# Performance work log

Hardware: AMD Instinct MI355X
Metric: run time of the kernel (lower is better)

The kernel has to match this reference:

```python
import jax, jax.numpy as jnp
import numpy as np

HEADS = 4


def _forward(x_atoms, pos, edge_attr, molecular_features, emb_W, emb_b, mp_W1, mp_b1, mp_W2, mp_b2, ln_g, ln_b, attn_in_w, attn_in_b, attn_out_w, attn_out_b, pool_W, pool_b, mol_gate, lrn_gate, molemb_W1, molemb_b1, molemb_W2, molemb_b2, lrnemb_W1, lrnemb_b1, lrnemb_W2, lrnemb_b2, fus_W1, fus_b1, fus_W2, fus_b2, head_W1, head_b1, head_W2, head_b2, edge_index, batch_idx):
    N = x_atoms.shape[0]
    B = molecular_features.shape[0]
    A = N // B  # equal-size molecules; batch_idx = repeat(arange(B), A)
    H = emb_W.shape[1]
    L = mp_W1.shape[0]
    src, dst = edge_index[0], edge_index[1]  # PyG: x_j = x[src], x_i = x[dst]
    x = x_atoms @ emb_W + emb_b
    # distance features (constant across layers)
    diff = pos[dst] - pos[src]
    d = jnp.sqrt(jnp.sum(diff * diff, axis=1, keepdims=True) + 1e-12)
    dist_feat = jnp.concatenate([d, 1.0 / (1.0 + d), jnp.exp(-d)], axis=1)  # [E,3]
    ones_e = jnp.ones((src.shape[0], 1), x.dtype)
    cnt = jnp.maximum(jax.ops.segment_sum(ones_e, dst, num_segments=N), 1.0)
    for l in range(L):
        res = x
        msg = jnp.concatenate([x[dst], x[src], dist_feat], axis=1)  # [E, 2H+3]
        msg = jax.nn.relu(msg @ mp_W1[l] + mp_b1[l]) @ mp_W2[l] + mp_b2[l]
        x = jax.ops.segment_sum(msg, dst, num_segments=N) / cnt  # mean aggregation
        y = x + res
        mu = y.mean(-1, keepdims=True)
        var = jnp.var(y, axis=-1, keepdims=True)
        x = (y - mu) * jax.lax.rsqrt(var + 1e-5) * ln_g[l] + ln_b[l]
    xm = x.reshape(B, A, H)
    explicit = xm.mean(axis=1)  # scatter_mean over equal-size graphs
    # per-molecule multi-head self-attention (torch MHA, eval mode)
    hd = H // HEADS
    qkv = xm @ attn_in_w.T + attn_in_b
    q, k, v = jnp.split(qkv, 3, axis=-1)
    q = q.reshape(B, A, HEADS, hd)
    k = k.reshape(B, A, HEADS, hd)
    v = v.reshape(B, A, HEADS, hd)
    scores = jnp.einsum('bqhd,bkhd->bhqk', q, k) / jnp.sqrt(jnp.asarray(hd, x.dtype))
    att = jax.nn.softmax(scores, axis=-1)
    o = jnp.einsum('bhqk,bkhd->bqhd', att, v).reshape(B, A, H)
    attended = o @ attn_out_w.T + attn_out_b
    aw = jax.nn.softmax(jnp.sum(attended * xm, axis=-1), axis=1)  # [B,A]
    wmean = jnp.sum(attended * aw[..., None], axis=1)
    maxp = attended.max(axis=1)
    meanp = attended.mean(axis=1)
    stdp = jnp.std(attended, axis=1, ddof=1)  # torch.std unbiased
    pooled = jnp.stack([wmean, maxp, meanp, stdp], axis=0)  # [4,B,H]
    proj = jnp.einsum('kbh,khf->kbf', pooled, pool_W) + pool_b[:, None, :]
    learned = jnp.moveaxis(proj, 0, 1).reshape(B, -1)  # [B,LF]
    # per-property gated MLPs, vectorized over P (atom gates are computed but unused in the source)
    gm = molecular_features[None] * jax.nn.sigmoid(mol_gate)[:, None, :]
    gl = learned[None] * jax.nn.sigmoid(lrn_gate)[:, None, :]
    molrep = jax.nn.relu(jnp.einsum('pbm,pmh->pbh', gm, molemb_W1) + molemb_b1[:, None, :])
    molrep = jnp.einsum('pbh,phk->pbk', molrep, molemb_W2) + molemb_b2[:, None, :]
    lrnrep = jax.nn.relu(jnp.einsum('pbm,pmh->pbh', gl, lrnemb_W1) + lrnemb_b1[:, None, :])
    lrnrep = jnp.einsum('pbh,phk->pbk', lrnrep, lrnemb_W2) + lrnemb_b2[:, None, :]
    P = mol_gate.shape[0]
    comb = jnp.concatenate([jnp.broadcast_to(explicit[None], (P, B, H)), molrep, lrnrep], axis=-1)
    fused = jax.nn.relu(jnp.einsum('pbc,pch->pbh', comb, fus_W1) + fus_b1[:, None, :])
    fused = jnp.einsum('pbh,phk->pbk', fused, fus_W2) + fus_b2[:, None, :]
    h = jax.nn.relu(jnp.einsum('pbh,phk->pbk', fused, head_W1) + head_b1[:, None, :])
    out = jnp.einsum('pbk,pko->pbo', h, head_W2) + head_b2[:, None, :]
    return out  # [P,B,1]: stacked predictions for the 4 properties


def setup_inputs() -> dict:
    key = jax.random.key(0)
    ks = jax.random.split(key, 24)
    B, A, F, M, H, LF, L, P = 1024, 32, 64, 200, 128, 64, 3, 4
    N = B * A
    E = N * 16
    H2, H4, Q = H // 2, H // 4, LF // 4
    n = lambda i, shape, s=1.0: jax.random.normal(ks[i], shape, dtype=jnp.float32) * s
    inp = {}
    inp['x_atoms'] = n(0, (N, F))
    inp['pos'] = n(1, (N, 3)) * 3.0
    inp['edge_attr'] = n(2, (E, 4))
    inp['molecular_features'] = n(3, (B, M))
    inp['emb_W'] = n(4, (F, H), 0.1)
    inp['emb_b'] = jnp.zeros((H,), jnp.float32)
    inp['mp_W1'] = n(5, (L, 2 * H + 3, H), 0.05)
    inp['mp_b1'] = jnp.zeros((L, H), jnp.float32)
    inp['mp_W2'] = n(6, (L, H, H), 0.05)
    inp['mp_b2'] = jnp.zeros((L, H), jnp.float32)
    inp['ln_g'] = jnp.ones((L, H), jnp.float32)
    inp['ln_b'] = jnp.zeros((L, H), jnp.float32)
    inp['attn_in_w'] = n(7, (3 * H, H), 0.08)
    inp['attn_in_b'] = jnp.zeros((3 * H,), jnp.float32)
    inp['attn_out_w'] = n(8, (H, H), 0.08)
    inp['attn_out_b'] = jnp.zeros((H,), jnp.float32)
    inp['pool_W'] = n(9, (4, H, Q), 0.08)
    inp['pool_b'] = jnp.zeros((4, Q), jnp.float32)
    inp['mol_gate'] = n(10, (P, M))
    inp['lrn_gate'] = n(11, (P, LF))
    inp['molemb_W1'] = n(12, (P, M, H2), 0.08)
    inp['molemb_b1'] = jnp.zeros((P, H2), jnp.float32)
    inp['molemb_W2'] = n(13, (P, H2, H2), 0.08)
    inp['molemb_b2'] = jnp.zeros((P, H2), jnp.float32)
    inp['lrnemb_W1'] = n(14, (P, LF, H2), 0.08)
    inp['lrnemb_b1'] = jnp.zeros((P, H2), jnp.float32)
    inp['lrnemb_W2'] = n(15, (P, H2, H2), 0.08)
    inp['lrnemb_b2'] = jnp.zeros((P, H2), jnp.float32)
    inp['fus_W1'] = n(16, (P, 2 * H, H), 0.08)
    inp['fus_b1'] = jnp.zeros((P, H), jnp.float32)
    inp['fus_W2'] = n(17, (P, H, H2), 0.08)
    inp['fus_b2'] = jnp.zeros((P, H2), jnp.float32)
    inp['head_W1'] = n(18, (P, H2, H4), 0.08)
    inp['head_b1'] = jnp.zeros((P, H4), jnp.float32)
    inp['head_W2'] = n(19, (P, H4, 1), 0.08)
    inp['head_b2'] = jnp.zeros((P, 1), jnp.float32)
    inp['edge_index'] = jax.random.randint(ks[20], (2, E), 0, N)
    inp['batch_idx'] = jnp.repeat(jnp.arange(B), A)
    return inp


def reference(x_atoms, pos, edge_attr, molecular_features, emb_W, emb_b, mp_W1, mp_b1, mp_W2, mp_b2, ln_g, ln_b, attn_in_w, attn_in_b, attn_out_w, attn_out_b, pool_W, pool_b, mol_gate, lrn_gate, molemb_W1, molemb_b1, molemb_W2, molemb_b2, lrnemb_W1, lrnemb_b1, lrnemb_W2, lrnemb_b2, fus_W1, fus_b1, fus_W2, fus_b2, head_W1, head_b1, head_W2, head_b2, edge_index, batch_idx):
    return _forward(x_atoms, pos, edge_attr, molecular_features, emb_W, emb_b, mp_W1, mp_b1, mp_W2, mp_b2, ln_g, ln_b, attn_in_w, attn_in_b, attn_out_w, attn_out_b, pool_W, pool_b, mol_gate, lrn_gate, molemb_W1, molemb_b1, molemb_W2, molemb_b2, lrnemb_W1, lrnemb_b1, lrnemb_W2, lrnemb_b2, fus_W1, fus_b1, fus_W2, fus_b2, head_W1, head_b1, head_W2, head_b2, edge_index, batch_idx)
```

## Files before the change

kernel.cpp:

```cpp
#include <hip/hip_runtime.h>

#define NE 524288
#define NN 32768
#define NB 1024

#define F4(p) (*(const float4*)(p))

typedef __bf16 bf16x8 __attribute__((ext_vector_type(8)));
typedef float  f32x4  __attribute__((ext_vector_type(4)));

__device__ __forceinline__ float sigmoidf_(float v) { return 1.f / (1.f + expf(-v)); }

__device__ __forceinline__ void bf16split(float f, short &hi, short &lo) {
  unsigned u = __float_as_uint(f);
  unsigned rh = (u + 0x7FFFu + ((u >> 16) & 1u)) >> 16;
  float fh = __uint_as_float(rh << 16);
  float fl = f - fh;
  unsigned u2 = __float_as_uint(fl);
  unsigned rl = (u2 + 0x7FFFu + ((u2 >> 16) & 1u)) >> 16;
  hi = (short)rh; lo = (short)rl;
}

__device__ __forceinline__ unsigned short f2bf(float f) {
  unsigned u = __float_as_uint(f);
  return (unsigned short)((u + 0x7FFFu + ((u >> 16) & 1u)) >> 16);
}
__device__ __forceinline__ float bf2f(unsigned short h) {
  return __uint_as_float(((unsigned)h) << 16);
}

__device__ __forceinline__ void ld32(float* xr, const float* p) {
#pragma unroll
  for (int i = 0; i < 32; i += 4) {
    float4 v = F4(&p[i]);
    xr[i] = v.x; xr[i+1] = v.y; xr[i+2] = v.z; xr[i+3] = v.w;
  }
}

__device__ __forceinline__ float dot32r(const float* __restrict__ w, const float* xr) {
  float s = 0.f;
#pragma unroll
  for (int i = 0; i < 32; i += 4) {
    float4 ww = F4(&w[i]);
    s = fmaf(xr[i],   ww.x, s);
    s = fmaf(xr[i+1], ww.y, s);
    s = fmaf(xr[i+2], ww.z, s);
    s = fmaf(xr[i+3], ww.w, s);
  }
  return s;
}

__global__ __launch_bounds__(256) void hist_kernel(const int* __restrict__ ei, int* __restrict__ cnt) {
  const int e = blockIdx.x*256 + threadIdx.x;
  atomicAdd(&cnt[ei[NE + e]], 1);
}

__global__ __launch_bounds__(1024) void scan_kernel(
    const int* __restrict__ cnt, int* __restrict__ off, int* __restrict__ cur)
{
  __shared__ int wsum[16];
  const int t = threadIdx.x;
  int local[32];
  const int base = t*32;
  int s = 0;
#pragma unroll
  for (int i = 0; i < 32; ++i) { local[i] = cnt[base+i]; s += local[i]; }
  int pre = s;
  const int lane = t & 63;
#pragma unroll
  for (int o = 1; o < 64; o <<= 1) { int v = __shfl_up(pre, o); if (lane >= o) pre += v; }
  if (lane == 63) wsum[t >> 6] = pre;
  __syncthreads();
  if (t == 0) { int a = 0; for (int w = 0; w < 16; ++w) { int v = wsum[w]; wsum[w] = a; a += v; } }
  __syncthreads();
  int excl = wsum[t >> 6] + pre - s;
#pragma unroll
  for (int i = 0; i < 32; ++i) { off[base+i] = excl; cur[base+i] = excl; excl += local[i]; }
  if (t == 1023) off[NN] = excl;
}

__global__ __launch_bounds__(256) void scatter_kernel(
    const float* __restrict__ pos, const int* __restrict__ ei,
    int* __restrict__ cur, float4* __restrict__ csr_rec)
{
  const int e = blockIdx.x*256 + threadIdx.x;
  const int s = ei[e];
  const int d = ei[NE + e];
  float dx = pos[d*3+0] - pos[s*3+0];
  float dy = pos[d*3+1] - pos[s*3+1];
  float dz = pos[d*3+2] - pos[s*3+2];
  float dist = sqrtf(dx*dx + dy*dy + dz*dz + 1e-12f);
  const int slot = atomicAdd(&cur[d], 1);
  csr_rec[slot] = make_float4(__int_as_float(s), dist, 1.f/(1.f + dist), expf(-dist));
}

__device__ __forceinline__ void pack_decode(int r, int N, int &k, int &n) {
  const int j = r & 7, lane = (r >> 3) & 63, rest = r >> 9;
  const int NT = N >> 4;
  const int t = rest % NT, kc = rest / NT;
  k = kc*32 + (lane >> 4)*8 + j;
  n = t*16 + (lane & 15);
}

#define W1AB_OFF 0
#define W2_OFF   98304
#define WIN_OFF  147456
#define WOUT_OFF 196608
#define EMB_OFF  212992
#define PK_TOTAL 221184

__global__ __launch_bounds__(256) void prep_kernel(
    const float* __restrict__ mp_W1, const float* __restrict__ mp_W2,
    const float* __restrict__ win, const float* __restrict__ wout,
    const float* __restrict__ emb_W, const float* __restrict__ mp_b1,
    short* __restrict__ bh, short* __restrict__ bl, float* __restrict__ pqbias)
{
  const int i = blockIdx.x*256 + threadIdx.x;
  if (i < 768) { const int l = i >> 8, t = i & 255; pqbias[i] = t < 128 ? mp_b1[l*128 + t] : 0.f; }
  if (i >= PK_TOTAL) return;
  int k, n; float v;
  if (i < W2_OFF) {
    const int l = i / 32768, r = i % 32768;
    pack_decode(r, 256, k, n);
    const float* W = mp_W1 + (size_t)l*259*128;
    v = (n < 128) ? W[k*128 + n] : W[(128+k)*128 + (n-128)];
  } else if (i < WIN_OFF) {
    const int q = i - W2_OFF, l = q / 16384, r = q % 16384;
    pack_decode(r, 128, k, n);
    v = mp_W2[(size_t)l*16384 + k*128 + n];
  } else if (i < WOUT_OFF) {
    pack_decode(i - WIN_OFF, 384, k, n);
    v = win[n*128 + k];
  } else if (i < EMB_OFF) {
    pack_decode(i - WOUT_OFF, 128, k, n);
    v = wout[n*128 + k];
  } else {
    pack_decode(i - EMB_OFF, 128, k, n);
    v = emb_W[k*128 + n];
  }
  short h_, lo; bf16split(v, h_, lo);
  bh[i] = h_; bl[i] = lo;
}

__global__ __launch_bounds__(256, 2) void mfma_gemm_kernel(
    const float* __restrict__ A, int lda, int K,
    const short* __restrict__ Bh, const short* __restrict__ Bl,
    const float* __restrict__ bias, float* __restrict__ C, int ncols, int ldc,
    int relu, unsigned short* __restrict__ qbf)
{
  const int lane = threadIdx.x & 63, wid = threadIdx.x >> 6;
  const int m0 = blockIdx.x * 128 + wid * 32;
  const int n0 = blockIdx.y * 64;
  const int NT = ncols >> 4;
  const int cl = lane & 15, kg = lane >> 4;
  const int KC = K >> 5;

  f32x4 acc[2][4];
#pragma unroll
  for (int s = 0; s < 2; ++s)
#pragma unroll
    for (int t = 0; t < 4; ++t) acc[s][t] = (f32x4){0.f,0.f,0.f,0.f};

  for (int kc = 0; kc < KC; ++kc) {
    bf16x8 Ah[2], Al[2];
#pragma unroll
    for (int s = 0; s < 2; ++s) {
      const float* ap = &A[(size_t)(m0 + s*16 + cl)*lda + kc*32 + kg*8];
      const float4 f0 = F4(ap), f1 = F4(ap + 4);
      const float fv[8] = {f0.x,f0.y,f0.z,f0.w,f1.x,f1.y,f1.z,f1.w};
      union { short s[8]; bf16x8 b; } uh, ul;
#pragma unroll
      for (int j = 0; j < 8; ++j) bf16split(fv[j], uh.s[j], ul.s[j]);
      Ah[s] = uh.b; Al[s] = ul.b;
    }
    bf16x8 Bfh[4], Bfl[4];
#pragma unroll
    for (int t = 0; t < 4; ++t) {
      const size_t off = (((size_t)(kc*NT + (n0 >> 4) + t))*64 + lane)*8;
      Bfh[t] = *(const bf16x8*)&Bh[off];
      Bfl[t] = *(const bf16x8*)&Bl[off];
    }
#pragma unroll
    for (int s = 0; s < 2; ++s)
#pragma unroll
      for (int t = 0; t < 4; ++t)
        acc[s][t] = __builtin_amdgcn_mfma_f32_16x16x32_bf16(Ah[s], Bfh[t], acc[s][t], 0, 0, 0);
#pragma unroll
    for (int s = 0; s < 2; ++s)
#pragma unroll
      for (int t = 0; t < 4; ++t)
        acc[s][t] = __builtin_amdgcn_mfma_f32_16x16x32_bf16(Ah[s], Bfl[t], acc[s][t], 0, 0, 0);
#pragma unroll
    for (int s = 0; s < 2; ++s)
#pragma unroll
      for (int t = 0; t < 4; ++t)
        acc[s][t] = __builtin_amdgcn_mfma_f32_16x16x32_bf16(Al[s], Bfh[t], acc[s][t], 0, 0, 0);
  }

#pragma unroll
  for (int t = 0; t < 4; ++t) {
    const int col = n0 + t*16 + cl;
    const float bv = bias[col];
#pragma unroll
    for (int s = 0; s < 2; ++s) {
      const int rbase = m0 + s*16 + kg*4;
#pragma unroll
      for (int r = 0; r < 4; ++r) {
        float v = acc[s][t][r] + bv;
        if (relu) v = fmaxf(v, 0.f);
        if (qbf && col >= 128)
          qbf[(size_t)(rbase + r)*128 + (col - 128)] = f2bf(v);
        else
          C[(size_t)(rbase + r)*ldc + col] = v;
      }
    }
  }
}

__global__ __launch_bounds__(256, 2) void mfma_gemm_ln_kernel(
    const float* __restrict__ A, int lda,
    const short* __restrict__ Bh, const short* __restrict__ Bl,
    const float* __restrict__ b2, const int* __restrict__ csr_off,
    const float* __restrict__ g, const float* __restrict__ bb,
    float* __restrict__ x)
{
  const int lane = threadIdx.x & 63, wid = threadIdx.x >> 6;
  const int m0 = blockIdx.x * 64 + wid * 16;
  const int cl = lane & 15, kg = lane >> 4;

  bf16x8 Ah[4], Al[4];
#pragma unroll
  for (int kc = 0; kc < 4; ++kc) {
    const float* ap = &A[(size_t)(m0 + cl)*lda + kc*32 + kg*8];
    const float4 f0 = F4(ap), f1 = F4(ap + 4);
    const float fv[8] = {f0.x,f0.y,f0.z,f0.w,f1.x,f1.y,f1.z,f1.w};
    union { short s[8]; bf16x8 b; } uh, ul;
#pragma unroll
    for (int j = 0; j < 8; ++j) bf16split(fv[j], uh.s[j], ul.s[j]);
    Ah[kc] = uh.b; Al[kc] = ul.b;
  }

  f32x4 acc[8];
#pragma unroll
  for (int t = 0; t < 8; ++t) acc[t] = (f32x4){0.f,0.f,0.f,0.f};

#pragma unroll
  for (int kc = 0; kc < 4; ++kc) {
    bf16x8 Bfh[8], Bfl[8];
#pragma unroll
    for (int t = 0; t < 8; ++t) {
      const size_t off = (((size_t)(kc*8 + t))*64 + lane)*8;
      Bfh[t] = *(const bf16x8*)&Bh[off];
      Bfl[t] = *(const bf16x8*)&Bl[off];
    }
#pragma unroll
    for (int t = 0; t < 8; ++t)
      acc[t] = __builtin_amdgcn_mfma_f32_16x16x32_bf16(Ah[kc], Bfh[t], acc[t], 0, 0, 0);
#pragma unroll
    for (int t = 0; t < 8; ++t)
      acc[t] = __builtin_amdgcn_mfma_f32_16x16x32_bf16(Ah[kc], Bfl[t], acc[t], 0, 0, 0);
#pragma unroll
    for (int t = 0; t < 8; ++t)
      acc[t] = __builtin_amdgcn_mfma_f32_16x16x32_bf16(Al[kc], Bfh[t], acc[t], 0, 0, 0);
  }

  const int r0 = m0 + kg*4;
  float sflag[4];
#pragma unroll
  for (int r = 0; r < 4; ++r)
    sflag[r] = (csr_off[r0 + r + 1] > csr_off[r0 + r]) ? 1.f : 0.f;

  float ps[4] = {0.f,0.f,0.f,0.f}, pq[4] = {0.f,0.f,0.f,0.f};
  float yv[8][4];
#pragma unroll
  for (int t = 0; t < 8; ++t) {
    const int col = t*16 + cl;
    const float b2v = b2[col];
#pragma unroll
    for (int r = 0; r < 4; ++r) {
      const float y = acc[t][r] + sflag[r]*b2v + x[(size_t)(r0 + r)*128 + col];
      yv[t][r] = y;
      ps[r] += y;
      pq[r] = fmaf(y, y, pq[r]);
    }
  }
#pragma unroll
  for (int o = 1; o < 16; o <<= 1) {
#pragma unroll
    for (int r = 0; r < 4; ++r) { ps[r] += __shfl_xor(ps[r], o); pq[r] += __shfl_xor(pq[r], o); }
  }
#pragma unroll
  for (int r = 0; r < 4; ++r) {
    const float mu = ps[r] * (1.f/128.f);
    const float var = pq[r]*(1.f/128.f) - mu*mu;
    const float rstd = rsqrtf(var + 1e-5f);
#pragma unroll
    for (int t = 0; t < 8; ++t) {
      const int col = t*16 + cl;
      x[(size_t)(r0 + r)*128 + col] = (yv[t][r] - mu)*rstd*g[col] + bb[col];
    }
  }
}

__global__ __launch_bounds__(256, 6) void agg_kernel(
    float* __restrict__ P, const unsigned short* __restrict__ Qbf,
    const int* __restrict__ csr_off, const float4* __restrict__ csr_rec,
    const float* __restrict__ W1)
{
  const int tid = threadIdx.x;
  const int node = blockIdx.x*4 + (tid >> 6);
  const int lane = tid & 63;
  const int c0 = lane*2;
  const int off0 = csr_off[node], off1 = csr_off[node+1];

  const float* __restrict__ w1c = W1 + 256*128;
  const float w00 = w1c[c0],       w01 = w1c[c0+1];
  const float w10 = w1c[128+c0],   w11 = w1c[128+c0+1];
  const float w20 = w1c[256+c0],   w21 = w1c[256+c0+1];
  const float2 p = *(const float2*)&P[(size_t)node*128 + c0];

  float a0 = 0.f, a1 = 0.f;
  int e = off0;
  for (; e + 8 <= off1; e += 8) {
    float4 rc[8];
#pragma unroll
    for (int j = 0; j < 8; ++j) rc[j] = csr_rec[e+j];
    ushort2 qv[8];
#pragma unroll
    for (int j = 0; j < 8; ++j)
      qv[j] = *(const ushort2*)&Qbf[(size_t)__float_as_int(rc[j].x)*128 + c0];
#pragma unroll
    for (int j = 0; j < 8; ++j) {
      float h0 = p.x + bf2f(qv[j].x);
      h0 = fmaf(rc[j].y, w00, h0); h0 = fmaf(rc[j].z, w10, h0); h0 = fmaf(rc[j].w, w20, h0);
      float h1 = p.y + bf2f(qv[j].y);
      h1 = fmaf(rc[j].y, w01, h1); h1 = fmaf(rc[j].z, w11, h1); h1 = fmaf(rc[j].w, w21, h1);
      a0 += fmaxf(h0, 0.f);
      a1 += fmaxf(h1, 0.f);
    }
  }
  for (; e < off1; ++e) {
    const float4 rc = csr_rec[e];
    const ushort2 qv = *(const ushort2*)&Qbf[(size_t)__float_as_int(rc.x)*128 + c0];
    float h0 = p.x + bf2f(qv.x);
    h0 = fmaf(rc.y, w00, h0); h0 = fmaf(rc.z, w10, h0); h0 = fmaf(rc.w, w20, h0);
    float h1 = p.y + bf2f(qv.y);
    h1 = fmaf(rc.y, w01, h1); h1 = fmaf(rc.z, w11, h1); h1 = fmaf(rc.w, w21, h1);
    a0 += fmaxf(h0, 0.f);
    a1 += fmaxf(h1, 0.f);
  }
  const int deg = off1 - off0;
  const float rc_ = deg > 0 ? 1.f/(float)deg : 1.f;
  *(float2*)&P[(size_t)node*128 + c0] = make_float2(a0*rc_, a1*rc_);
}

__global__ __launch_bounds__(128) void attn_kernel(float* __restrict__ dqkv)
{
  __shared__ float sk[32*132];
  __shared__ float sv[32*132];
  const int tid = threadIdx.x;
  const int b = blockIdx.x;

  for (int idx = tid; idx < 1024; idx += 128) {
    const int a = idx >> 5, c4 = idx & 31;
    *(float4*)&sk[a*132 + c4*4] = F4(&dqkv[(size_t)(b*32+a)*384 + 128 + c4*4]);
    *(float4*)&sv[a*132 + c4*4] = F4(&dqkv[(size_t)(b*32+a)*384 + 256 + c4*4]);
  }
  __syncthreads();

  const int h = tid >> 5, qr = tid & 31;
  float qreg[32];
  ld32(qreg, &dqkv[(size_t)(b*32+qr)*384 + h*32]);

  float sc[32];
#pragma unroll
  for (int k = 0; k < 32; ++k)
    sc[k] = dot32r(&sk[k*132 + h*32], qreg) * 0.17677669529663687f;
  float mx = sc[0];
#pragma unroll
  for (int k = 1; k < 32; ++k) mx = fmaxf(mx, sc[k]);
  float se = 0.f;
#pragma unroll
  for (int k = 0; k < 32; ++k) { sc[k] = expf(sc[k] - mx); se += sc[k]; }
  const float inv = 1.f / se;

  __syncthreads();

  float od[32];
#pragma unroll
  for (int i = 0; i < 32; ++i) od[i] = 0.f;
#pragma unroll 4
  for (int k = 0; k < 32; ++k) {
    const float w = sc[k] * inv;
    const float* vr = &sv[k*132 + h*32];
#pragma unroll
    for (int i = 0; i < 32; i += 4) {
      float4 v = F4(&vr[i]);
      od[i]   = fmaf(w, v.x, od[i]);
      od[i+1] = fmaf(w, v.y, od[i+1]);
      od[i+2] = fmaf(w, v.z, od[i+2]);
      od[i+3] = fmaf(w, v.w, od[i+3]);
    }
  }
#pragma unroll
  for (int i = 0; i < 32; i += 4)
    *(float4*)&sk[qr*132 + h*32 + i] = make_float4(od[i], od[i+1], od[i+2], od[i+3]);
  __syncthreads();

  for (int idx = tid; idx < 1024; idx += 128) {
    const int a = idx >> 5, c4 = idx & 31;
    *(float4*)&dqkv[(size_t)(b*32+a)*384 + 256 + c4*4] = F4(&sk[a*132 + c4*4]);
  }
}

__global__ __launch_bounds__(128) void pool_kernel(
    const float* __restrict__ att, const float* __restrict__ x,
    const float* __restrict__ pW, const float* __restrict__ pb,
    float* __restrict__ expl, float* __restrict__ lrn)
{
  __shared__ float satt[32*132];
  __shared__ float sx[32*132];
  __shared__ float aw_l[32];
  __shared__ float spool[512];
  const int tid = threadIdx.x;
  const int b = blockIdx.x;

  for (int idx = tid; idx < 1024; idx += 128) {
    const int a = idx >> 5, c4 = idx & 31;
    *(float4*)&satt[a*132 + c4*4] = F4(&att[(size_t)(b*32+a)*128 + c4*4]);
    *(float4*)&sx[a*132 + c4*4]   = F4(&x[(size_t)(b*32+a)*128 + c4*4]);
  }
  __syncthreads();

  {
    const int a = tid >> 2, q4 = tid & 3;
    float sp = 0.f;
#pragma unroll
    for (int i = 0; i < 32; ++i)
      sp = fmaf(satt[a*132 + q4*32 + i], sx[a*132 + q4*32 + i], sp);
    sp += __shfl_xor(sp, 1);
    sp += __shfl_xor(sp, 2);
    if (q4 == 0) aw_l[a] = sp;
  }
  __syncthreads();

  {
    float awr[32];
    float mxl = aw_l[0];
#pragma unroll
    for (int a = 1; a < 32; ++a) mxl = fmaxf(mxl, aw_l[a]);
    float se = 0.f;
#pragma unroll
    for (int a = 0; a < 32; ++a) { awr[a] = expf(aw_l[a] - mxl); se += awr[a]; }
    const float inv = 1.f / se;
    const int c = tid;
    float mx = -3.4e38f, sm = 0.f, wm = 0.f, ex = 0.f;
#pragma unroll
    for (int a = 0; a < 32; ++a) {
      const float v = satt[a*132 + c];
      mx = fmaxf(mx, v);
      sm += v;
      wm = fmaf(v, awr[a], wm);
      ex += sx[a*132 + c];
    }
    wm *= inv;
    const float mean = sm * 0.03125f;
    float s2 = 0.f;
#pragma unroll
    for (int a = 0; a < 32; ++a) {
      const float d = satt[a*132 + c] - mean;
      s2 = fmaf(d, d, s2);
    }
    const float stdp = sqrtf(s2 * (1.f/31.f));
    expl[b*128 + c] = ex * 0.03125f;
    spool[c]       = wm;
    spool[128 + c] = mx;
    spool[256 + c] = mean;
    spool[384 + c] = stdp;
  }
  __syncthreads();

  if (tid < 64) {
    const int k = tid >> 4, qq = tid & 15;
    const float* pk = pW + k*2048;
    float s0 = 0.f, s1 = 0.f, s2 = 0.f, s3 = 0.f;
    for (int h2 = 0; h2 < 128; h2 += 4) {
      s0 = fmaf(spool[k*128 + h2],   pk[h2*16 + qq],     s0);
      s1 = fmaf(spool[k*128 + h2+1], pk[(h2+1)*16 + qq], s1);
      s2 = fmaf(spool[k*128 + h2+2], pk[(h2+2)*16 + qq], s2);
      s3 = fmaf(spool[k*128 + h2+3], pk[(h2+3)*16 + qq], s3);
    }
    lrn[b*64 + tid] = pb[k*16 + qq] + (s0+s1) + (s2+s3);
  }
}

__global__ __launch_bounds__(256) void fused_head_kernel(
    const float* __restrict__ molf, const float* __restrict__ lrn,
    const float* __restrict__ expl,
    const float* __restrict__ mol_gate, const float* __restrict__ lrn_gate,
    const float* __restrict__ meW1, const float* __restrict__ meb1,
    const float* __restrict__ meW2, const float* __restrict__ meb2,
    const float* __restrict__ leW1, const float* __restrict__ leb1,
    const float* __restrict__ leW2, const float* __restrict__ leb2,
    const float* __restrict__ fW1, const float* __restrict__ fb1,
    const float* __restrict__ fW2, const float* __restrict__ fb2,
    const float* __restrict__ hW1, const float* __restrict__ hb1,
    const float* __restrict__ hW2, const float* __restrict__ hb2,
    float* __restrict__ out)
{
  const int p  = blockIdx.y;
  const int b0 = blockIdx.x * 32;
  const int t  = threadIdx.x;
  const int m  = t >> 3, hg = t & 7;

  __shared__ float sgm[32][201];
  __shared__ float sgl[32][65];
  __shared__ float smr[32][65];
  __shared__ float slr[32][65];
  __shared__ float scomb[32][257];
  __shared__ float sf1[32][129];
  __shared__ float sf2[32][65];

  for (int i = t; i < 32*200; i += 256) {
    const int mm = i / 200, k = i - mm*200;
    sgm[mm][k] = molf[(size_t)(b0+mm)*200 + k] * sigmoidf_(mol_gate[p*200 + k]);
  }
  for (int i = t; i < 32*64; i += 256) {
    const int mm = i >> 6, k = i & 63;
    sgl[mm][k] = lrn[(size_t)(b0+mm)*64 + k] * sigmoidf_(lrn_gate[p*64 + k]);
  }
  for (int i = t; i < 32*128; i += 256) {
    const int mm = i >> 7, c = i & 127;
    scomb[mm][c] = expl[(size_t)(b0+mm)*128 + c];
  }
  __syncthreads();

  {
    const float* w = meW1 + p*12800;
    const int h0 = hg*8;
    float acc[8] = {0.f,0.f,0.f,0.f,0.f,0.f,0.f,0.f};
    for (int k = 0; k < 200; ++k) {
      const float a = sgm[m][k];
      const float4 w0 = F4(&w[k*64 + h0]);
      const float4 w1 = F4(&w[k*64 + h0 + 4]);
      acc[0] = fmaf(a, w0.x, acc[0]); acc[1] = fmaf(a, w0.y, acc[1]);
      acc[2] = fmaf(a, w0.z, acc[2]); acc[3] = fmaf(a, w0.w, acc[3]);
      acc[4] = fmaf(a, w1.x, acc[4]); acc[5] = fmaf(a, w1.y, acc[5]);
      acc[6] = fmaf(a, w1.z, acc[6]); acc[7] = fmaf(a, w1.w, acc[7]);
    }
#pragma unroll
    for (int j = 0; j < 8; ++j)
      smr[m][h0+j] = fmaxf(acc[j] + meb1[p*64 + h0 + j], 0.f);
  }
  {
    const float* w = leW1 + p*4096;
    const int h0 = hg*8;
    float acc[8] = {0.f,0.f,0.f,0.f,0.f,0.f,0.f,0.f};
    for (int k = 0; k < 64; ++k) {
      const float a = sgl[m][k];
      const float4 w0 = F4(&w[k*64 + h0]);
      const float4 w1 = F4(&w[k*64 + h0 + 4]);
      acc[0] = fmaf(a, w0.x, acc[0]); acc[1] = fmaf(a, w0.y, acc[1]);
      acc[2] = fmaf(a, w0.z, acc[2]); acc[3] = fmaf(a, w0.w, acc[3]);
      acc[4] = fmaf(a, w1.x, acc[4]); acc[5] = fmaf(a, w1.y, acc[5]);
      acc[6] = fmaf(a, w1.z, acc[6]); acc[7] = fmaf(a, w1.w, acc[7]);
    }
#pragma unroll
    for (int j = 0; j < 8; ++j)
      slr[m][h0+j] = fmaxf(acc[j] + leb1[p*64 + h0 + j], 0.f);
  }
  __syncthreads();

  {
    const float* w  = meW2 + p*4096;
    const float* w2 = leW2 + p*4096;
    const int h0 = hg*8;
    float acc[8] = {0.f,0.f,0.f,0.f,0.f,0.f,0.f,0.f};
    float bcc[8] = {0.f,0.f,0.f,0.f,0.f,0.f,0.f,0.f};
    for (int k = 0; k < 64; ++k) {
      const float a = smr[m][k];
      const float b = slr[m][k];
      const float4 w0 = F4(&w[k*64 + h0]);
      const float4 w1 = F4(&w[k*64 + h0 + 4]);
      const float4 v0 = F4(&w2[k*64 + h0]);
      const float4 v1 = F4(&w2[k*64 + h0 + 4]);
      acc[0] = fmaf(a, w0.x, acc[0]); acc[1] = fmaf(a, w0.y, acc[1]);
      acc[2] = fmaf(a, w0.z, acc[2]); acc[3] = fmaf(a, w0.w, acc[3]);
      acc[4] = fmaf(a, w1.x, acc[4]); acc[5] = fmaf(a, w1.y, acc[5]);
      acc[6] = fmaf(a, w1.z, acc[6]); acc[7] = fmaf(a, w1.w, acc[7]);
      bcc[0] = fmaf(b, v0.x, bcc[0]); bcc[1] = fmaf(b, v0.y, bcc[1]);
      bcc[2] = fmaf(b, v0.z, bcc[2]); bcc[3] = fmaf(b, v0.w, bcc[3]);
      bcc[4] = fmaf(b, v1.x, bcc[4]); bcc[5] = fmaf(b, v1.y, bcc[5]);
      bcc[6] = fmaf(b, v1.z, bcc[6]); bcc[7] = fmaf(b, v1.w, bcc[7]);
    }
#pragma unroll
    for (int j = 0; j < 8; ++j) {
      scomb[m][128 + h0 + j] = acc[j] + meb2[p*64 + h0 + j];
      scomb[m][192 + h0 + j] = bcc[j] + leb2[p*64 + h0 + j];
    }
  }
  __syncthreads();

  {
    const float* w = fW1 + p*32768;
    const int h0 = hg*16;
    float acc[16];
#pragma unroll
    for (int j = 0; j < 16; ++j) acc[j] = 0.f;
    for (int k = 0; k < 256; ++k) {
      const float a = scomb[m][k];
      const float* wp = &w[k*128 + h0];
#pragma unroll
      for (int j = 0; j < 16; j += 4) {
        const float4 wv = F4(&wp[j]);
        acc[j]   = fmaf(a, wv.x, acc[j]);
        acc[j+1] = fmaf(a, wv.y, acc[j+1]);
        acc[j+2] = fmaf(a, wv.z, acc[j+2]);
        acc[j+3] = fmaf(a, wv.w, acc[j+3]);
      }
    }
#pragma unroll
    for (int j = 0; j < 16; ++j)
      sf1[m][h0+j] = fmaxf(acc[j] + fb1[p*128 + h0 + j], 0.f);
  }
  __syncthreads();

  {
    const float* w = fW2 + p*8192;
    const int h0 = hg*8;
    float acc[8] = {0.f,0.f,0.f,0.f,0.f,0.f,0.f,0.f};
    for (int k = 0; k < 128; ++k) {
      const float a = sf1[m][k];
      const float4 w0 = F4(&w[k*64 + h0]);
      const float4 w1 = F4(&w[k*64 + h0 + 4]);
      acc[0] = fmaf(a, w0.x, acc[0]); acc[1] = fmaf(a, w0.y, acc[1]);
      acc[2] = fmaf(a, w0.z, acc[2]); acc[3] = fmaf(a, w0.w, acc[3]);
      acc[4] = fmaf(a, w1.x, acc[4]); acc[5] = fmaf(a, w1.y, acc[5]);
      acc[6] = fmaf(a, w1.z, acc[6]); acc[7] = fmaf(a, w1.w, acc[7]);
    }
#pragma unroll
    for (int j = 0; j < 8; ++j)
      sf2[m][h0+j] = acc[j] + fb2[p*64 + h0 + j];
  }
  __syncthreads();

  {
    const float* w = hW1 + p*2048;
    const int h0 = hg*4;
    float acc[4] = {0.f,0.f,0.f,0.f};
    for (int k = 0; k < 64; ++k) {
      const float a = sf2[m][k];
      const float4 w0 = F4(&w[k*32 + h0]);
      acc[0] = fmaf(a, w0.x, acc[0]); acc[1] = fmaf(a, w0.y, acc[1]);
      acc[2] = fmaf(a, w0.z, acc[2]); acc[3] = fmaf(a, w0.w, acc[3]);
    }
    float val = 0.f;
#pragma unroll
    for (int j = 0; j < 4; ++j)
      val = fmaf(fmaxf(acc[j] + hb1[p*32 + h0 + j], 0.f), hW2[p*32 + h0 + j], val);
    val += __shfl_xor(val, 1);
    val += __shfl_xor(val, 2);
    val += __shfl_xor(val, 4);
    if (hg == 0) out[p*1024 + b0 + m] = val + hb2[p];
  }
}

extern "C" void kernel_launch(void* const* d_in, const int* in_sizes, int n_in,
                              void* d_out, int out_size, void* d_ws, size_t ws_size,
                              hipStream_t stream) {
  const float* x_atoms    = (const float*)d_in[0];
  const float* pos        = (const float*)d_in[1];
  const float* molf       = (const float*)d_in[3];
  const float* emb_W      = (const float*)d_in[4];
  const float* emb_b      = (const float*)d_in[5];
  const float* mp_W1      = (const float*)d_in[6];
  const float* mp_b1      = (const float*)d_in[7];
  const float* mp_W2      = (const float*)d_in[8];
  const float* mp_b2      = (const float*)d_in[9];
  const float* ln_g       = (const float*)d_in[10];
  const float* ln_b       = (const float*)d_in[11];
  const float* attn_in_w  = (const float*)d_in[12];
  const float* attn_in_b  = (const float*)d_in[13];
  const float* attn_out_w = (const float*)d_in[14];
  const float* attn_out_b = (const float*)d_in[15];
  const float* pool_W     = (const float*)d_in[16];
  const float* pool_b     = (const float*)d_in[17];
  const float* mol_gate   = (const float*)d_in[18];
  const float* lrn_gate   = (const float*)d_in[19];
  const float* meW1       = (const float*)d_in[20];
  const float* meb1       = (const float*)d_in[21];
  const float* meW2       = (const float*)d_in[22];
  const float* meb2       = (const float*)d_in[23];
  const float* leW1       = (const float*)d_in[24];
  const float* leb1       = (const float*)d_in[25];
  const float* leW2       = (const float*)d_in[26];
  const float* leb2       = (const float*)d_in[27];
  const float* fW1        = (const float*)d_in[28];
  const float* fb1        = (const float*)d_in[29];
  const float* fW2        = (const float*)d_in[30];
  const float* fb2        = (const float*)d_in[31];
  const float* hW1        = (const float*)d_in[32];
  const float* hb1        = (const float*)d_in[33];
  const float* hW2        = (const float*)d_in[34];
  const float* hb2        = (const float*)d_in[35];
  const int*   ei         = (const int*)d_in[36];

  float* ws      = (float*)d_ws;
  float* x       = ws;
  float* region  = x + (size_t)NN*128;
  float* P       = region;
  unsigned short* Qbf = (unsigned short*)(region + (size_t)NN*128);
  float* dqkv    = region;
  float* att     = region + (size_t)NN*384;
  float* csr_rf  = att + (size_t)NN*128;
  float4* csr_rec = (float4*)csr_rf;
  int*   cnt_i   = (int*)(csr_rf + (size_t)NE*4);
  int*   csr_off = cnt_i + NN;
  int*   cur     = csr_off + NN + 64;
  float* lrn     = (float*)(cur + NN);
  float* expl    = lrn + NB*64;
  float* pqbias  = expl + NB*128;
  short* bh      = (short*)(pqbias + 768);
  short* bl      = bh + PK_TOTAL;

  hipMemsetAsync(cnt_i, 0, (size_t)NN*sizeof(int), stream);

  prep_kernel<<<(PK_TOTAL + 255)/256, 256, 0, stream>>>(
      mp_W1, mp_W2, attn_in_w, attn_out_w, emb_W, mp_b1, bh, bl, pqbias);
  hist_kernel<<<NE/256, 256, 0, stream>>>(ei, cnt_i);
  scan_kernel<<<1, 1024, 0, stream>>>(cnt_i, csr_off, cur);
  scatter_kernel<<<NE/256, 256, 0, stream>>>(pos, ei, cur, csr_rec);

  mfma_gemm_kernel<<<dim3(NN/128, 2), 256, 0, stream>>>(
      x_atoms, 64, 64, bh + EMB_OFF, bl + EMB_OFF, emb_b, x, 128, 128, 0, nullptr);

  for (int l = 0; l < 3; ++l) {
    mfma_gemm_kernel<<<dim3(NN/128, 4), 256, 0, stream>>>(
        x, 128, 128, bh + W1AB_OFF + l*32768, bl + W1AB_OFF + l*32768,
        pqbias + l*256, P, 256, 128, 0, Qbf);
    agg_kernel<<<NN/4, 256, 0, stream>>>(P, Qbf, csr_off, csr_rec,
                                         mp_W1 + (size_t)l*259*128);
    mfma_gemm_ln_kernel<<<NN/64, 256, 0, stream>>>(
        P, 128, bh + W2_OFF + l*16384, bl + W2_OFF + l*16384,
        mp_b2 + l*128, csr_off, ln_g + l*128, ln_b + l*128, x);
  }

  mfma_gemm_kernel<<<dim3(NN/128, 6), 256, 0, stream>>>(
      x, 128, 128, bh + WIN_OFF, bl + WIN_OFF, attn_in_b, dqkv, 384, 384, 0, nullptr);
  attn_kernel<<<NB, 128, 0, stream>>>(dqkv);
  mfma_gemm_kernel<<<dim3(NN/128, 2), 256, 0, stream>>>(
      dqkv + 256, 384, 128, bh + WOUT_OFF, bl + WOUT_OFF, attn_out_b, att, 128, 128, 0, nullptr);
  pool_kernel<<<NB, 128, 0, stream>>>(att, x, pool_W, pool_b, expl, lrn);

  fused_head_kernel<<<dim3(32, 4), 256, 0, stream>>>(
      molf, lrn, expl, mol_gate, lrn_gate,
      meW1, meb1, meW2, meb2, leW1, leb1, leW2, leb2,
      fW1, fb1, fW2, fb2, hW1, hb1, hW2, hb2, (float*)d_out);
}
```

Measured before the change: 447.1 us.

## Restructure head MLP kernel to four molecules per 64-thread block

Replaces the head MLP kernel, which used 32 molecules per 256-thread block, with one handling 4 molecules per 64-thread block. Activations are stored interleaved by molecule so each thread computes one output feature for all four molecules. This launches many more blocks to fill the GPU's compute units. In exchange, the weight matrices are re-read by more blocks through L2.

```diff
diff --git a/kernel.cpp b/kernel.cpp
--- a/kernel.cpp
+++ b/kernel.cpp
@@ -494,7 +494,7 @@
   }
 }
 
-__global__ __launch_bounds__(256) void fused_head_kernel(
+__global__ __launch_bounds__(64) void head4_kernel(
     const float* __restrict__ molf, const float* __restrict__ lrn,
     const float* __restrict__ expl,
     const float* __restrict__ mol_gate, const float* __restrict__ lrn_gate,
@@ -508,160 +508,143 @@
     const float* __restrict__ hW2, const float* __restrict__ hb2,
     float* __restrict__ out)
 {
-  const int p  = blockIdx.y;
-  const int b0 = blockIdx.x * 32;
-  const int t  = threadIdx.x;
-  const int m  = t >> 3, hg = t & 7;
-
-  __shared__ float sgm[32][201];
-  __shared__ float sgl[32][65];
-  __shared__ float smr[32][65];
-  __shared__ float slr[32][65];
-  __shared__ float scomb[32][257];
-  __shared__ float sf1[32][129];
-  __shared__ float sf2[32][65];
-
-  for (int i = t; i < 32*200; i += 256) {
+  const int p = blockIdx.y, b0 = blockIdx.x*4, t = threadIdx.x;
+  __shared__ float sgm[200*4];
+  __shared__ float sgl[64*4];
+  __shared__ float smr[64*4];
+  __shared__ float slr[64*4];
+  __shared__ float scomb[256*4];
+  __shared__ float sf1[128*4];
+  __shared__ float sf2[64*4];
+
+  for (int i = t; i < 800; i += 64) {
     const int mm = i / 200, k = i - mm*200;
-    sgm[mm][k] = molf[(size_t)(b0+mm)*200 + k] * sigmoidf_(mol_gate[p*200 + k]);
-  }
-  for (int i = t; i < 32*64; i += 256) {
+    sgm[k*4 + mm] = molf[(size_t)(b0+mm)*200 + k] * sigmoidf_(mol_gate[p*200 + k]);
+  }
+  for (int i = t; i < 256; i += 64) {
     const int mm = i >> 6, k = i & 63;
-    sgl[mm][k] = lrn[(size_t)(b0+mm)*64 + k] * sigmoidf_(lrn_gate[p*64 + k]);
-  }
-  for (int i = t; i < 32*128; i += 256) {
-    const int mm = i >> 7, c = i & 127;
-    scomb[mm][c] = expl[(size_t)(b0+mm)*128 + c];
+    sgl[k*4 + mm] = lrn[(size_t)(b0+mm)*64 + k] * sigmoidf_(lrn_gate[p*64 + k]);
+  }
+  for (int i = t; i < 512; i += 64) {
+    const int c = i >> 2, mm = i & 3;
+    scomb[i] = expl[(size_t)(b0+mm)*128 + c];
   }
   __syncthreads();
 
   {
-    const float* w = meW1 + p*12800;
-    const int h0 = hg*8;
-    float acc[8] = {0.f,0.f,0.f,0.f,0.f,0.f,0.f,0.f};
+    const float* w = meW1 + p*12800 + t;
+    float a0=0.f,a1=0.f,a2=0.f,a3=0.f;
+#pragma unroll 4
     for (int k = 0; k < 200; ++k) {
-      const float a = sgm[m][k];
-      const float4 w0 = F4(&w[k*64 + h0]);
-      const float4 w1 = F4(&w[k*64 + h0 + 4]);
-      acc[0] = fmaf(a, w0.x, acc[0]); acc[1] = fmaf(a, w0.y, acc[1]);
-      acc[2] = fmaf(a, w0.z, acc[2]); acc[3] = fmaf(a, w0.w, acc[3]);
-      acc[4] = fmaf(a, w1.x, acc[4]); acc[5] = fmaf(a, w1.y, acc[5]);
-      acc[6] = fmaf(a, w1.z, acc[6]); acc[7] = fmaf(a, w1.w, acc[7]);
-    }
-#pragma unroll
-    for (int j = 0; j < 8; ++j)
-      smr[m][h0+j] = fmaxf(acc[j] + meb1[p*64 + h0 + j], 0.f);
+      const float wv = w[k*64];
+      const float4 a = F4(&sgm[k*4]);
+      a0=fmaf(a.x,wv,a0); a1=fmaf(a.y,wv,a1); a2=fmaf(a.z,wv,a2); a3=fmaf(a.w,wv,a3);
+    }
+    const float b = meb1[p*64 + t];
+    smr[t*4+0]=fmaxf(a0+b,0.f); smr[t*4+1]=fmaxf(a1+b,0.f);
+    smr[t*4+2]=fmaxf(a2+b,0.f); smr[t*4+3]=fmaxf(a3+b,0.f);
   }
   {
-    const float* w = leW1 + p*4096;
-    const int h0 = hg*8;
-    float acc[8] = {0.f,0.f,0.f,0.f,0.f,0.f,0.f,0.f};
+    const float* w = leW1 + p*4096 + t;
+    float a0=0.f,a1=0.f,a2=0.f,a3=0.f;
+#pragma unroll 4
     for (int k = 0; k < 64; ++k) {
-      const float a = sgl[m][k];
-      const float4 w0 = F4(&w[k*64 + h0]);
-      const float4 w1 = F4(&w[k*64 + h0 + 4]);
-      acc[0] = fmaf(a, w0.x, acc[0]); acc[1] = fmaf(a, w0.y, acc[1]);
-      acc[2] = fmaf(a, w0.z, acc[2]); acc[3] = fmaf(a, w0.w, acc[3]);
-      acc[4] = fmaf(a, w1.x, acc[4]); acc[5] = fmaf(a, w1.y, acc[5]);
-      acc[6] = fmaf(a, w1.z, acc[6]); acc[7] = fmaf(a, w1.w, acc[7]);
-    }
-#pragma unroll
-    for (int j = 0; j < 8; ++j)
-      slr[m][h0+j] = fmaxf(acc[j] + leb1[p*64 + h0 + j], 0.f);
+      const float wv = w[k*64];
+      const float4 a = F4(&sgl[k*4]);
+      a0=fmaf(a.x,wv,a0); a1=fmaf(a.y,wv,a1); a2=fmaf(a.z,wv,a2); a3=fmaf(a.w,wv,a3);
+    }
+    const float b = leb1[p*64 + t];
+    slr[t*4+0]=fmaxf(a0+b,0.f); slr[t*4+1]=fmaxf(a1+b,0.f);
+    slr[t*4+2]=fmaxf(a2+b,0.f); slr[t*4+3]=fmaxf(a3+b,0.f);
   }
   __syncthreads();
 
   {
-    const float* w  = meW2 + p*4096;
-    const float* w2 = leW2 + p*4096;
-    const int h0 = hg*8;
-    float acc[8] = {0.f,0.f,0.f,0.f,0.f,0.f,0.f,0.f};
-    float bcc[8] = {0.f,0.f,0.f,0.f,0.f,0.f,0.f,0.f};
+    const float* w  = meW2 + p*4096 + t;
+    const float* w2 = leW2 + p*4096 + t;
+    float a0=0.f,a1=0.f,a2=0.f,a3=0.f;
+    float c0=0.f,c1=0.f,c2=0.f,c3=0.f;
+#pragma unroll 2
     for (int k = 0; k < 64; ++k) {
-      const float a = smr[m][k];
-      const float b = slr[m][k];
-      const float4 w0 = F4(&w[k*64 + h0]);
-      const float4 w1 = F4(&w[k*64 + h0 + 4]);
-      const float4 v0 = F4(&w2[k*64 + h0]);
-      const float4 v1 = F4(&w2[k*64 + h0 + 4]);
-      acc[0] = fmaf(a, w0.x, acc[0]); acc[1] = fmaf(a, w0.y, acc[1]);
-      acc[2] = fmaf(a, w0.z, acc[2]); acc[3] = fmaf(a, w0.w, acc[3]);
-      acc[4] = fmaf(a, w1.x, acc[4]); acc[5] = fmaf(a, w1.y, acc[5]);
-      acc[6] = fmaf(a, w1.z, acc[6]); acc[7] = fmaf(a, w1.w, acc[7]);
-      bcc[0] = fmaf(b, v0.x, bcc[0]); bcc[1] = fmaf(b, v0.y, bcc[1]);
-      bcc[2] = fmaf(b, v0.z, bcc[2]); bcc[3] = fmaf(b, v0.w, bcc[3]);
-      bcc[4] = fmaf(b, v1.x, bcc[4]); bcc[5] = fmaf(b, v1.y, bcc[5]);
-      bcc[6] = fmaf(b, v1.z, bcc[6]); bcc[7] = fmaf(b, v1.w, bcc[7]);
-    }
-#pragma unroll
-    for (int j = 0; j < 8; ++j) {
-      scomb[m][128 + h0 + j] = acc[j] + meb2[p*64 + h0 + j];
-      scomb[m][192 + h0 + j] = bcc[j] + leb2[p*64 + h0 + j];
-    }
+      const float wv = w[k*64];
+      const float4 a = F4(&smr[k*4]);
+      a0=fmaf(a.x,wv,a0); a1=fmaf(a.y,wv,a1); a2=fmaf(a.z,wv,a2); a3=fmaf(a.w,wv,a3);
+      const float vv = w2[k*64];
+      const float4 b = F4(&slr[k*4]);
+      c0=fmaf(b.x,vv,c0); c1=fmaf(b.y,vv,c1); c2=fmaf(b.z,vv,c2); c3=fmaf(b.w,vv,c3);
+    }
+    const float bm = meb2[p*64 + t], bl_ = leb2[p*64 + t];
+    scomb[(128+t)*4+0]=a0+bm; scomb[(128+t)*4+1]=a1+bm;
+    scomb[(128+t)*4+2]=a2+bm; scomb[(128+t)*4+3]=a3+bm;
+    scomb[(192+t)*4+0]=c0+bl_; scomb[(192+t)*4+1]=c1+bl_;
+    scomb[(192+t)*4+2]=c2+bl_; scomb[(192+t)*4+3]=c3+bl_;
   }
   __syncthreads();
 
   {
     const float* w = fW1 + p*32768;
-    const int h0 = hg*16;
-    float acc[16];
-#pragma unroll
-    for (int j = 0; j < 16; ++j) acc[j] = 0.f;
+    float a0=0.f,a1=0.f,a2=0.f,a3=0.f;
+    float c0=0.f,c1=0.f,c2=0.f,c3=0.f;
+#pragma unroll 2
     for (int k = 0; k < 256; ++k) {
-      const float a = scomb[m][k];
-      const float* wp = &w[k*128 + h0];
-#pragma unroll
-      for (int j = 0; j < 16; j += 4) {
-        const float4 wv = F4(&wp[j]);
-        acc[j]   = fmaf(a, wv.x, acc[j]);
-        acc[j+1] = fmaf(a, wv.y, acc[j+1]);
-        acc[j+2] = fmaf(a, wv.z, acc[j+2]);
-        acc[j+3] = fmaf(a, wv.w, acc[j+3]);
+      const float4 a = F4(&scomb[k*4]);
+      const float w0 = w[k*128 + t];
+      const float w1 = w[k*128 + 64 + t];
+      a0=fmaf(a.x,w0,a0); a1=fmaf(a.y,w0,a1); a2=fmaf(a.z,w0,a2); a3=fmaf(a.w,w0,a3);
+      c0=fmaf(a.x,w1,c0); c1=fmaf(a.y,w1,c1); c2=fmaf(a.z,w1,c2); c3=fmaf(a.w,w1,c3);
+    }
+    const float b0_ = fb1[p*128 + t], b1_ = fb1[p*128 + 64 + t];
+    sf1[t*4+0]=fmaxf(a0+b0_,0.f); sf1[t*4+1]=fmaxf(a1+b0_,0.f);
+    sf1[t*4+2]=fmaxf(a2+b0_,0.f); sf1[t*4+3]=fmaxf(a3+b0_,0.f);
+    sf1[(t+64)*4+0]=fmaxf(c0+b1_,0.f); sf1[(t+64)*4+1]=fmaxf(c1+b1_,0.f);
+    sf1[(t+64)*4+2]=fmaxf(c2+b1_,0.f); sf1[(t+64)*4+3]=fmaxf(c3+b1_,0.f);
+  }
+  __syncthreads();
+
+  {
+    const float* w = fW2 + p*8192 + t;
+    float a0=0.f,a1=0.f,a2=0.f,a3=0.f;
+#pragma unroll 4
+    for (int k = 0; k < 128; ++k) {
+      const float wv = w[k*64];
+      const float4 a = F4(&sf1[k*4]);
+      a0=fmaf(a.x,wv,a0); a1=fmaf(a.y,wv,a1); a2=fmaf(a.z,wv,a2); a3=fmaf(a.w,wv,a3);
+    }
+    const float b = fb2[p*64 + t];
+    sf2[t*4+0]=a0+b; sf2[t*4+1]=a1+b; sf2[t*4+2]=a2+b; sf2[t*4+3]=a3+b;
+  }
+  __syncthreads();
+
+  {
+    float a0=0.f,a1=0.f,a2=0.f,a3=0.f;
+    if (t < 32) {
+      const float* w = hW1 + p*2048 + t;
+#pragma unroll 4
+      for (int k = 0; k < 64; ++k) {
+        const float wv = w[k*32];
+        const float4 a = F4(&sf2[k*4]);
+        a0=fmaf(a.x,wv,a0); a1=fmaf(a.y,wv,a1); a2=fmaf(a.z,wv,a2); a3=fmaf(a.w,wv,a3);
       }
-    }
-#pragma unroll
-    for (int j = 0; j < 16; ++j)
-      sf1[m][h0+j] = fmaxf(acc[j] + fb1[p*128 + h0 + j], 0.f);
-  }
-  __syncthreads();
-
-  {
-    const float* w = fW2 + p*8192;
-    const int h0 = hg*8;
-    float acc[8] = {0.f,0.f,0.f,0.f,0.f,0.f,0.f,0.f};
-    for (int k = 0; k < 128; ++k) {
-      const float a = sf1[m][k];
-      const float4 w0 = F4(&w[k*64 + h0]);
-      const float4 w1 = F4(&w[k*64 + h0 + 4]);
-      acc[0] = fmaf(a, w0.x, acc[0]); acc[1] = fmaf(a, w0.y, acc[1]);
-      acc[2] = fmaf(a, w0.z, acc[2]); acc[3] = fmaf(a, w0.w, acc[3]);
-      acc[4] = fmaf(a, w1.x, acc[4]); acc[5] = fmaf(a, w1.y, acc[5]);
-      acc[6] = fmaf(a, w1.z, acc[6]); acc[7] = fmaf(a, w1.w, acc[7]);
-    }
-#pragma unroll
-    for (int j = 0; j < 8; ++j)
-      sf2[m][h0+j] = acc[j] + fb2[p*64 + h0 + j];
-  }
-  __syncthreads();
-
-  {
-    const float* w = hW1 + p*2048;
-    const int h0 = hg*4;
-    float acc[4] = {0.f,0.f,0.f,0.f};
-    for (int k = 0; k < 64; ++k) {
-      const float a = sf2[m][k];
-      const float4 w0 = F4(&w[k*32 + h0]);
-      acc[0] = fmaf(a, w0.x, acc[0]); acc[1] = fmaf(a, w0.y, acc[1]);
-      acc[2] = fmaf(a, w0.z, acc[2]); acc[3] = fmaf(a, w0.w, acc[3]);
-    }
-    float val = 0.f;
-#pragma unroll
-    for (int j = 0; j < 4; ++j)
-      val = fmaf(fmaxf(acc[j] + hb1[p*32 + h0 + j], 0.f), hW2[p*32 + h0 + j], val);
-    val += __shfl_xor(val, 1);
-    val += __shfl_xor(val, 2);
-    val += __shfl_xor(val, 4);
-    if (hg == 0) out[p*1024 + b0 + m] = val + hb2[p];
+      const float hb = hb1[p*32 + t], w2v = hW2[p*32 + t];
+      a0 = fmaxf(a0+hb,0.f)*w2v;
+      a1 = fmaxf(a1+hb,0.f)*w2v;
+      a2 = fmaxf(a2+hb,0.f)*w2v;
+      a3 = fmaxf(a3+hb,0.f)*w2v;
+    }
+#pragma unroll
+    for (int o = 1; o < 32; o <<= 1) {
+      a0 += __shfl_xor(a0, o);
+      a1 += __shfl_xor(a1, o);
+      a2 += __shfl_xor(a2, o);
+      a3 += __shfl_xor(a3, o);
+    }
+    if (t == 0) {
+      const float hb2v = hb2[p];
+      out[p*1024 + b0 + 0] = a0 + hb2v;
+      out[p*1024 + b0 + 1] = a1 + hb2v;
+      out[p*1024 + b0 + 2] = a2 + hb2v;
+      out[p*1024 + b0 + 3] = a3 + hb2v;
+    }
   }
 }
 
@@ -752,7 +735,7 @@
       dqkv + 256, 384, 128, bh + WOUT_OFF, bl + WOUT_OFF, attn_out_b, att, 128, 128, 0, nullptr);
   pool_kernel<<<NB, 128, 0, stream>>>(att, x, pool_W, pool_b, expl, lrn);
 
-  fused_head_kernel<<<dim3(32, 4), 256, 0, stream>>>(
+  head4_kernel<<<dim3(NB/4, 4), 64, 0, stream>>>(
       molf, lrn, expl, mol_gate, lrn_gate,
       meW1, meb1, meW2, meb2, leW1, leb1, leW2, leb2,
       fW1, fb1, fW2, fb2, hW1, hb1, hW2, hb2, (float*)d_out);
```

Measured after the change: 432.9 us. 1.03x faster.
